# Kernel tuning notes

Hardware: AMD Instinct MI355X
Metric: run time of the kernel (lower is better)

Reference implementation:

```python
import jax, jax.numpy as jnp
import numpy as np

N_NODES = 50000
N_EDGES = 800000
IN_FEATS = 128
HIDDEN = 128
NUM_CLASSES = 47


def setup_inputs() -> dict:
    key = jax.random.key(0)
    k1, k2, k3, k4 = jax.random.split(key, 4)
    features = jax.random.normal(k1, (N_NODES, IN_FEATS), dtype=jnp.float32)
    edge_index = jax.random.randint(k2, (2, N_EDGES), 0, N_NODES, dtype=jnp.int32)
    # Glorot-style init for weights, zeros for bias (DGL GraphConv defaults)
    W1 = jax.random.normal(k3, (IN_FEATS, HIDDEN), dtype=jnp.float32) * (1.0 / np.sqrt(IN_FEATS))
    b1 = jnp.zeros((HIDDEN,), dtype=jnp.float32)
    W2 = jax.random.normal(k4, (HIDDEN, NUM_CLASSES), dtype=jnp.float32) * (1.0 / np.sqrt(HIDDEN))
    b2 = jnp.zeros((NUM_CLASSES,), dtype=jnp.float32)
    return {"features": features, "edge_index": edge_index,
            "W1": W1, "b1": b1, "W2": W2, "b2": b2}


def _graph_conv(x, W, b, src, dst, norm_src, norm_dst, n_nodes):
    # DGL GraphConv, norm='both': D_dst^{-1/2} A D_src^{-1/2} (X W) + b
    h = (x * norm_src[:, None]) @ W            # transform before aggregation
    agg = jax.ops.segment_sum(h[src], dst, num_segments=n_nodes)
    return agg * norm_dst[:, None] + b


def reference(features, edge_index, W1, b1, W2, b2):
    src, dst = edge_index[0], edge_index[1]
    n = features.shape[0]
    ones = jnp.ones((src.shape[0],), dtype=features.dtype)
    deg_out = jax.ops.segment_sum(ones, src, num_segments=n)
    deg_in = jax.ops.segment_sum(ones, dst, num_segments=n)
    norm_src = jax.lax.rsqrt(jnp.clip(deg_out, 1.0))   # d_out^{-1/2}, clamp >= 1
    norm_dst = jax.lax.rsqrt(jnp.clip(deg_in, 1.0))    # d_in^{-1/2}, clamp >= 1

    h = _graph_conv(features, W1, b1, src, dst, norm_src, norm_dst, n)
    h = jax.nn.relu(h)
    out = _graph_conv(h, W2, b2, src, dst, norm_src, norm_dst, n)
    return out
```

## Files before the change

### kernel.cpp

```cpp
#include <hip/hip_runtime.h>
#include <hip/hip_fp16.h>

#define N_NODES 50000
#define N_EDGES 800000
#define IN_F 128
#define HID 128
#define NCLS 47
#define H2S 48
#define W2C 64
#define NCH 196
#define TM 32
#define XTS 40
#define NB 64
#define CHUNK 12500
#define PDW 12500
#define HHALF 6250
#define FQ 3125
#define NHIST 256
#define MEGA_LDS 25088


struct __align__(8)  h2x2 { __half2 a, b; };
struct __align__(16) h2x4 { __half2 a, b, c, d; };

__global__ __launch_bounds__(256) void mega1_kernel(const int* __restrict__ ei,
                                                    unsigned int* __restrict__ Pdst,
                                                    unsigned int* __restrict__ Psrc,
                                                    const float* __restrict__ X,
                                                    const float* __restrict__ W1,
                                                    __half* __restrict__ H1h) {
    extern __shared__ __align__(16) char smem[];
    const int t = threadIdx.x;
    if (blockIdx.x < NHIST) {
        unsigned int* h = (unsigned int*)smem;
        const int job = blockIdx.x;
        const bool is_src = job >= NHIST / 2;
        const int half = (job >> 6) & 1;
        const int chunk = job & (NB - 1);
        const int* ids = is_src ? ei : ei + N_EDGES;
        uint2* h2 = (uint2*)h;
        for (int j = t; j < HHALF / 2; j += 256) h2[j] = make_uint2(0u, 0u);
        __syncthreads();
        const int e0 = chunk * CHUNK;
        const int lo = half * HHALF;
        for (int k = t; k < CHUNK; k += 256) {
            int v = ids[e0 + k];
            int rel = (v >> 2) - lo;
            if ((unsigned)rel < HHALF)
                atomicAdd(&h[rel], 1u << ((v & 3) * 8));
        }
        __syncthreads();
        unsigned int* P = (is_src ? Psrc : Pdst) + (size_t)chunk * PDW + lo;
        uint2* P2 = (uint2*)P;
        for (int j = t; j < HHALF / 2; j += 256) P2[j] = h2[j];
    } else {
        float* xs = (float*)smem;
        const int row0 = (blockIdx.x - NHIST) * TM;
#pragma unroll
        for (int i = 0; i < 4; ++i) {
            int id = t + 256 * i;
            int r = id & 31;
            int q = id >> 5;
            int row = row0 + r;
            float4 v = make_float4(0.f, 0.f, 0.f, 0.f);
            if (row < N_NODES) v = *(const float4*)&X[(size_t)row * IN_F + 4 * q];
            xs[(4 * q + 0) * XTS + r] = v.x;
            xs[(4 * q + 1) * XTS + r] = v.y;
            xs[(4 * q + 2) * XTS + r] = v.z;
            xs[(4 * q + 3) * XTS + r] = v.w;
        }
        __syncthreads();
        const int c = t & 31;
        const int rg = t >> 5;
        float acc[4][4] = {{0.f}};
#pragma unroll 4
        for (int k = 0; k < IN_F; ++k) {
            const float4 w4 = *(const float4*)&W1[k * HID + 4 * c];
            const float4 a4 = *(const float4*)&xs[k * XTS + 4 * rg];
            const float wv[4] = {w4.x, w4.y, w4.z, w4.w};
            const float av[4] = {a4.x, a4.y, a4.z, a4.w};
#pragma unroll
            for (int i = 0; i < 4; ++i)
#pragma unroll
                for (int j = 0; j < 4; ++j)
                    acc[i][j] += av[i] * wv[j];
        }
#pragma unroll
        for (int i = 0; i < 4; ++i) {
            int row = row0 + 4 * rg + i;
            if (row < N_NODES) {
                h2x2 p = {__floats2half2_rn(acc[i][0], acc[i][1]),
                          __floats2half2_rn(acc[i][2], acc[i][3])};
                *(h2x2*)&H1h[(size_t)row * HID + 4 * c] = p;
            }
        }
    }
}

__global__ __launch_bounds__(256) void reduce_kernel(unsigned int* __restrict__ Pdst,
                                                     const unsigned int* __restrict__ Psrc,
                                                     int* __restrict__ cnt_in,
                                                     float* __restrict__ norm_src,
                                                     float* __restrict__ norm_dst,
                                                     int* __restrict__ chunk_sums) {
    __shared__ int sm[256];
    const int t = threadIdx.x;
    const int j = blockIdx.x * 256 + t;
    int tot = 0;
    if (j < PDW) {
        unsigned int run = 0;
        for (int b = 0; b < NB; ++b) {
            unsigned int v = Pdst[(size_t)b * PDW + j];
            Pdst[(size_t)b * PDW + j] = run;
            run += v;
        }
        int n0 = run & 0xff, n1 = (run >> 8) & 0xff;
        int n2 = (run >> 16) & 0xff, n3 = (run >> 24) & 0xff;
        *(int4*)&cnt_in[4 * j] = make_int4(n0, n1, n2, n3);
        *(float4*)&norm_dst[4 * j] = make_float4(
            rsqrtf(fmaxf((float)n0, 1.0f)), rsqrtf(fmaxf((float)n1, 1.0f)),
            rsqrtf(fmaxf((float)n2, 1.0f)), rsqrtf(fmaxf((float)n3, 1.0f)));
        tot = n0 + n1 + n2 + n3;
        unsigned int rs = 0;
        for (int b = 0; b < NB; ++b) rs += Psrc[(size_t)b * PDW + j];
        int s0 = rs & 0xff, s1 = (rs >> 8) & 0xff;
        int s2 = (rs >> 16) & 0xff, s3 = (rs >> 24) & 0xff;
        *(float4*)&norm_src[4 * j] = make_float4(
            rsqrtf(fmaxf((float)s0, 1.0f)), rsqrtf(fmaxf((float)s1, 1.0f)),
            rsqrtf(fmaxf((float)s2, 1.0f)), rsqrtf(fmaxf((float)s3, 1.0f)));
    }
    sm[t] = tot;
    __syncthreads();
    const int g = t & 63;
    for (int off = 32; off > 0; off >>= 1) {
        if (g < off) sm[t] += sm[t + off];
        __syncthreads();
    }
    if (g == 0) chunk_sums[blockIdx.x * 4 + (t >> 6)] = sm[t];
}

__global__ __launch_bounds__(256) void scan3_kernel(const int* __restrict__ cnt_in,
                                                    const int* __restrict__ chunk_sums,
                                                    int* __restrict__ offsets,
                                                    const float* __restrict__ W2,
                                                    float* __restrict__ W2p) {
    __shared__ int sm[256];
    const int t = threadIdx.x;
    int v = (t < NCH) ? chunk_sums[t] : 0;
    sm[t] = v;
    __syncthreads();
    for (int off = 1; off < 256; off <<= 1) {
        int u = (t >= off) ? sm[t - off] : 0;
        __syncthreads();
        sm[t] += u;
        __syncthreads();
    }
    const int basev = (blockIdx.x == 0) ? 0 : sm[blockIdx.x - 1];
    __syncthreads();
    const int idx = blockIdx.x * 256 + t;
    int c = (idx < N_NODES) ? cnt_in[idx] : 0;
    sm[t] = c;
    __syncthreads();
    for (int off = 1; off < 256; off <<= 1) {
        int u = (t >= off) ? sm[t - off] : 0;
        __syncthreads();
        sm[t] += u;
        __syncthreads();
    }
    if (idx < N_NODES) offsets[idx] = basev + sm[t] - c;
    if (blockIdx.x == 0) {
        if (t == 0) offsets[N_NODES] = N_EDGES;
        for (int i2 = t; i2 < HID * W2C; i2 += 256) {
            int k = i2 >> 6, cc = i2 & 63;
            W2p[i2] = (cc < NCLS) ? W2[k * NCLS + cc] : 0.f;
        }
    }
}

__global__ __launch_bounds__(256) void fill_kernel(const int* __restrict__ src,
                                                   const int* __restrict__ dst,
                                                   const int* __restrict__ offsets,
                                                   const unsigned int* __restrict__ Pdst,
                                                   int* __restrict__ csr_src) {
    __shared__ unsigned int cur[FQ];
    const int quarter = blockIdx.x >> 6;
    const int chunk = blockIdx.x & (NB - 1);
    for (int j = threadIdx.x; j < FQ; j += 256) cur[j] = 0u;
    __syncthreads();
    const unsigned int* base = Pdst + (size_t)chunk * PDW;
    const int e0 = chunk * CHUNK;
    const int lo = quarter * FQ;
    for (int k = threadIdx.x; k < CHUNK; k += 256) {
        int d = dst[e0 + k];
        int rel = (d >> 2) - lo;
        if ((unsigned)rel < FQ) {
            const int sh = (d & 3) * 8;
            unsigned int old = atomicAdd(&cur[rel], 1u << sh);
            unsigned int rank = (old >> sh) & 0xffu;
            unsigned int bh = (base[d >> 2] >> sh) & 0xffu;
            csr_src[offsets[d] + (int)bh + (int)rank] = src[e0 + k];
        }
    }
}

__global__ __launch_bounds__(256) void gather1_kernel(const __half* __restrict__ H1h,
        const int* __restrict__ offsets, const int* __restrict__ csr_src,
        const float* __restrict__ b1, const float* __restrict__ norm_src,
        const float* __restrict__ norm_dst, __half* __restrict__ Hrelu16) {
    const int lane = threadIdx.x & 63;
    const int q = lane >> 4;
    const int fl = lane & 15;
    const int row = blockIdx.x * 4 + (threadIdx.x >> 6);
    const int beg = offsets[row], end = offsets[row + 1];
    float a0 = 0.f, a1 = 0.f, a2 = 0.f, a3 = 0.f;
    float a4 = 0.f, a5 = 0.f, a6 = 0.f, a7 = 0.f;
    for (int base = beg; base < end; base += 64) {
        int idx = 0;
        float nsv = 0.f;
        if (base + lane < end) {
            idx = csr_src[base + lane];
            nsv = norm_src[idx];
        }
        const int cnt = min(end - base, 64);
        for (int j = 0; j < cnt; j += 16) {
            int e0 = j + q, e1 = j + 4 + q, e2 = j + 8 + q, e3 = j + 12 + q;
            int s0 = __shfl(idx, e0);  float n0 = __shfl(nsv, e0);
            int s1 = __shfl(idx, e1);  float n1 = __shfl(nsv, e1);
            int s2 = __shfl(idx, e2);  float n2 = __shfl(nsv, e2);
            int s3 = __shfl(idx, e3);  float n3 = __shfl(nsv, e3);
            h2x4 v0 = *(const h2x4*)&H1h[(size_t)s0 * HID + 8 * fl];
            h2x4 v1 = *(const h2x4*)&H1h[(size_t)s1 * HID + 8 * fl];
            h2x4 v2 = *(const h2x4*)&H1h[(size_t)s2 * HID + 8 * fl];
            h2x4 v3 = *(const h2x4*)&H1h[(size_t)s3 * HID + 8 * fl];
            float2 f;
            f = __half22float2(v0.a); a0 = fmaf(f.x, n0, a0); a1 = fmaf(f.y, n0, a1);
            f = __half22float2(v0.b); a2 = fmaf(f.x, n0, a2); a3 = fmaf(f.y, n0, a3);
            f = __half22float2(v0.c); a4 = fmaf(f.x, n0, a4); a5 = fmaf(f.y, n0, a5);
            f = __half22float2(v0.d); a6 = fmaf(f.x, n0, a6); a7 = fmaf(f.y, n0, a7);
            f = __half22float2(v1.a); a0 = fmaf(f.x, n1, a0); a1 = fmaf(f.y, n1, a1);
            f = __half22float2(v1.b); a2 = fmaf(f.x, n1, a2); a3 = fmaf(f.y, n1, a3);
            f = __half22float2(v1.c); a4 = fmaf(f.x, n1, a4); a5 = fmaf(f.y, n1, a5);
            f = __half22float2(v1.d); a6 = fmaf(f.x, n1, a6); a7 = fmaf(f.y, n1, a7);
            f = __half22float2(v2.a); a0 = fmaf(f.x, n2, a0); a1 = fmaf(f.y, n2, a1);
            f = __half22float2(v2.b); a2 = fmaf(f.x, n2, a2); a3 = fmaf(f.y, n2, a3);
            f = __half22float2(v2.c); a4 = fmaf(f.x, n2, a4); a5 = fmaf(f.y, n2, a5);
            f = __half22float2(v2.d); a6 = fmaf(f.x, n2, a6); a7 = fmaf(f.y, n2, a7);
            f = __half22float2(v3.a); a0 = fmaf(f.x, n3, a0); a1 = fmaf(f.y, n3, a1);
            f = __half22float2(v3.b); a2 = fmaf(f.x, n3, a2); a3 = fmaf(f.y, n3, a3);
            f = __half22float2(v3.c); a4 = fmaf(f.x, n3, a4); a5 = fmaf(f.y, n3, a5);
            f = __half22float2(v3.d); a6 = fmaf(f.x, n3, a6); a7 = fmaf(f.y, n3, a7);
        }
    }
    a0 += __shfl_xor(a0, 16); a1 += __shfl_xor(a1, 16);
    a2 += __shfl_xor(a2, 16); a3 += __shfl_xor(a3, 16);
    a4 += __shfl_xor(a4, 16); a5 += __shfl_xor(a5, 16);
    a6 += __shfl_xor(a6, 16); a7 += __shfl_xor(a7, 16);
    a0 += __shfl_xor(a0, 32); a1 += __shfl_xor(a1, 32);
    a2 += __shfl_xor(a2, 32); a3 += __shfl_xor(a3, 32);
    a4 += __shfl_xor(a4, 32); a5 += __shfl_xor(a5, 32);
    a6 += __shfl_xor(a6, 32); a7 += __shfl_xor(a7, 32);
    if (lane < 16) {
        float nd = norm_dst[row], ns = norm_src[row];
        float4 bA = *(const float4*)&b1[8 * fl];
        float4 bB = *(const float4*)&b1[8 * fl + 4];
        float o0 = fmaxf(fmaf(a0, nd, bA.x), 0.f) * ns;
        float o1 = fmaxf(fmaf(a1, nd, bA.y), 0.f) * ns;
        float o2 = fmaxf(fmaf(a2, nd, bA.z), 0.f) * ns;
        float o3 = fmaxf(fmaf(a3, nd, bA.w), 0.f) * ns;
        float o4 = fmaxf(fmaf(a4, nd, bB.x), 0.f) * ns;
        float o5 = fmaxf(fmaf(a5, nd, bB.y), 0.f) * ns;
        float o6 = fmaxf(fmaf(a6, nd, bB.z), 0.f) * ns;
        float o7 = fmaxf(fmaf(a7, nd, bB.w), 0.f) * ns;
        h2x4 p = {__floats2half2_rn(o0, o1), __floats2half2_rn(o2, o3),
                  __floats2half2_rn(o4, o5), __floats2half2_rn(o6, o7)};
        *(h2x4*)&Hrelu16[(size_t)row * HID + 8 * fl] = p;
    }
}

__global__ __launch_bounds__(128) void gemm2_kernel(const __half* __restrict__ Hrelu16,
                                                    const float* __restrict__ W2p,
                                                    __half* __restrict__ H2h) {
    __shared__ __align__(16) float xs[HID * XTS];
    const int t = threadIdx.x;
    const int row0 = blockIdx.x * TM;
#pragma unroll
    for (int i = 0; i < 4; ++i) {
        int id = t + 128 * i;
        int r = id & 31;
        int g = id >> 5;
        int row = row0 + r;
        h2x4 v{};
        if (row < N_NODES) v = *(const h2x4*)&Hrelu16[(size_t)row * HID + 8 * g];
        float2 f0 = __half22float2(v.a), f1 = __half22float2(v.b);
        float2 f2 = __half22float2(v.c), f3 = __half22float2(v.d);
        xs[(8 * g + 0) * XTS + r] = f0.x;
        xs[(8 * g + 1) * XTS + r] = f0.y;
        xs[(8 * g + 2) * XTS + r] = f1.x;
        xs[(8 * g + 3) * XTS + r] = f1.y;
        xs[(8 * g + 4) * XTS + r] = f2.x;
        xs[(8 * g + 5) * XTS + r] = f2.y;
        xs[(8 * g + 6) * XTS + r] = f3.x;
        xs[(8 * g + 7) * XTS + r] = f3.y;
    }
    __syncthreads();
    const int c = t & 15;
    const int rg = t >> 4;
    float acc[4][4] = {{0.f}};
#pragma unroll 4
    for (int k = 0; k < HID; ++k) {
        const float4 w4 = *(const float4*)&W2p[k * W2C + 4 * c];
        const float4 a4 = *(const float4*)&xs[k * XTS + 4 * rg];
        const float wv[4] = {w4.x, w4.y, w4.z, w4.w};
        const float av[4] = {a4.x, a4.y, a4.z, a4.w};
#pragma unroll
        for (int i = 0; i < 4; ++i)
#pragma unroll
            for (int j = 0; j < 4; ++j)
                acc[i][j] += av[i] * wv[j];
    }
    if (c < 12) {
#pragma unroll
        for (int i = 0; i < 4; ++i) {
            int row = row0 + 4 * rg + i;
            if (row < N_NODES) {
                h2x2 p = {__floats2half2_rn(acc[i][0], acc[i][1]),
                          __floats2half2_rn(acc[i][2], acc[i][3])};
                *(h2x2*)&H2h[(size_t)row * H2S + 4 * c] = p;
            }
        }
    }
}

__global__ __launch_bounds__(256) void gather2_kernel(const __half* __restrict__ H2h,
        const int* __restrict__ offsets, const int* __restrict__ csr_src,
        const float* __restrict__ b2, const float* __restrict__ norm_dst,
        float* __restrict__ out) {
    const int lane = threadIdx.x & 63;
    const int row = blockIdx.x * 4 + (threadIdx.x >> 6);
    const int beg = offsets[row], end = offsets[row + 1];
    const int cl = min(lane, H2S - 1);
    float acc = 0.f;
    for (int base = beg; base < end; base += 64) {
        int idx = 0;
        float wv = 0.f;
        if (base + lane < end) {
            idx = csr_src[base + lane];
            wv = 1.f;
        }
        const int cnt = min(end - base, 64);
        for (int j = 0; j < cnt; j += 4) {
            int s0 = __shfl(idx, j);     float w0 = __shfl(wv, j);
            int s1 = __shfl(idx, j + 1); float w1 = __shfl(wv, j + 1);
            int s2 = __shfl(idx, j + 2); float w2 = __shfl(wv, j + 2);
            int s3 = __shfl(idx, j + 3); float w3 = __shfl(wv, j + 3);
            float f0 = __half2float(H2h[(size_t)s0 * H2S + cl]);
            float f1 = __half2float(H2h[(size_t)s1 * H2S + cl]);
            float f2 = __half2float(H2h[(size_t)s2 * H2S + cl]);
            float f3 = __half2float(H2h[(size_t)s3 * H2S + cl]);
            acc = fmaf(f0, w0, acc);
            acc = fmaf(f1, w1, acc);
            acc = fmaf(f2, w2, acc);
            acc = fmaf(f3, w3, acc);
        }
    }
    if (lane < NCLS) out[(size_t)row * NCLS + lane] = acc * norm_dst[row] + b2[lane];
}

extern "C" void kernel_launch(void* const* d_in, const int* in_sizes, int n_in,
                              void* d_out, int out_size, void* d_ws, size_t ws_size,
                              hipStream_t stream) {
    const float* X  = (const float*)d_in[0];
    const int*   ei = (const int*)d_in[1];
    const float* W1 = (const float*)d_in[2];
    const float* b1 = (const float*)d_in[3];
    const float* W2 = (const float*)d_in[4];
    const float* b2 = (const float*)d_in[5];
    float* out = (float*)d_out;

    const int* src = ei;
    const int* dst = ei + N_EDGES;

    char* w = (char*)d_ws;
    auto alloc = [&](size_t bytes) {
        char* p = w;
        w += (bytes + 255) & ~(size_t)255;
        return p;
    };
    float*  norm_src   = (float*)alloc(N_NODES * 4);
    float*  norm_dst   = (float*)alloc(N_NODES * 4);
    int*    cnt_in     = (int*)alloc(N_NODES * 4);
    int*    offsets    = (int*)alloc((N_NODES + 1) * 4);
    int*    csr_src    = (int*)alloc((size_t)N_EDGES * 4);
    int*    chunk_sums = (int*)alloc(NCH * 4);
    float*  W2p        = (float*)alloc((size_t)HID * W2C * 4);
    __half* H1h        = (__half*)alloc((size_t)N_NODES * HID * 2);
    __half* Hrelu16    = (__half*)alloc((size_t)N_NODES * HID * 2);
    __half* H2h        = (__half*)alloc((size_t)N_NODES * H2S * 2);
    unsigned int* Pdst = (unsigned int*)alloc((size_t)NB * PDW * 4);
    unsigned int* Psrc = (unsigned int*)alloc((size_t)NB * PDW * 4);

    const int gemm_blocks = (N_NODES + TM - 1) / TM;
    mega1_kernel<<<NHIST + gemm_blocks, 256, MEGA_LDS, stream>>>(ei, Pdst, Psrc,
                                                                 X, W1, H1h);
    reduce_kernel<<<(PDW + 255) / 256, 256, 0, stream>>>(Pdst, Psrc, cnt_in,
                                                         norm_src, norm_dst, chunk_sums);
    scan3_kernel<<<NCH, 256, 0, stream>>>(cnt_in, chunk_sums, offsets, W2, W2p);
    fill_kernel<<<4 * NB, 256, 0, stream>>>(src, dst, offsets, Pdst, csr_src);

    gather1_kernel<<<N_NODES / 4, 256, 0, stream>>>(H1h, offsets, csr_src, b1,
                                                    norm_src, norm_dst, Hrelu16);
    gemm2_kernel<<<gemm_blocks, 128, 0, stream>>>(Hrelu16, W2p, H2h);
    gather2_kernel<<<N_NODES / 4, 256, 0, stream>>>(H2h, offsets, csr_src, b2,
                                                    norm_dst, out);
}
```

Measured before the change: 240.8 us.

## Co-schedule GEMM1 with CSR fill instead of histogram, widen histogram blocks

Moves the first dense GEMM (X·W1 to fp16) out of the fused histogram kernel and into the CSR fill kernel, so the GEMM blocks run alongside the atomic-heavy fill phase instead of the histogram phase. The histogram becomes its own kernel using 512-thread blocks with static LDS. The aim is to better hide the latency-bound fill scatter behind compute and to let the short histogram launch finish faster. The risk is that fill blocks queued alongside many GEMM blocks may be delayed, and the fill kernel's LDS footprint grows to 20 KB.

```diff
diff --git a/kernel.cpp b/kernel.cpp
--- a/kernel.cpp
+++ b/kernel.cpp
@@ -17,84 +17,37 @@
 #define HHALF 6250
 #define FQ 3125
 #define NHIST 256
-#define MEGA_LDS 25088
+#define FG_LDS 20480
 
 
 struct __align__(8)  h2x2 { __half2 a, b; };
 struct __align__(16) h2x4 { __half2 a, b, c, d; };
 
-__global__ __launch_bounds__(256) void mega1_kernel(const int* __restrict__ ei,
-                                                    unsigned int* __restrict__ Pdst,
-                                                    unsigned int* __restrict__ Psrc,
-                                                    const float* __restrict__ X,
-                                                    const float* __restrict__ W1,
-                                                    __half* __restrict__ H1h) {
-    extern __shared__ __align__(16) char smem[];
+__global__ __launch_bounds__(512) void hist_kernel(const int* __restrict__ ei,
+                                                   unsigned int* __restrict__ Pdst,
+                                                   unsigned int* __restrict__ Psrc) {
+    __shared__ unsigned int h[HHALF];
     const int t = threadIdx.x;
-    if (blockIdx.x < NHIST) {
-        unsigned int* h = (unsigned int*)smem;
-        const int job = blockIdx.x;
-        const bool is_src = job >= NHIST / 2;
-        const int half = (job >> 6) & 1;
-        const int chunk = job & (NB - 1);
-        const int* ids = is_src ? ei : ei + N_EDGES;
-        uint2* h2 = (uint2*)h;
-        for (int j = t; j < HHALF / 2; j += 256) h2[j] = make_uint2(0u, 0u);
-        __syncthreads();
-        const int e0 = chunk * CHUNK;
-        const int lo = half * HHALF;
-        for (int k = t; k < CHUNK; k += 256) {
-            int v = ids[e0 + k];
-            int rel = (v >> 2) - lo;
-            if ((unsigned)rel < HHALF)
-                atomicAdd(&h[rel], 1u << ((v & 3) * 8));
-        }
-        __syncthreads();
-        unsigned int* P = (is_src ? Psrc : Pdst) + (size_t)chunk * PDW + lo;
-        uint2* P2 = (uint2*)P;
-        for (int j = t; j < HHALF / 2; j += 256) P2[j] = h2[j];
-    } else {
-        float* xs = (float*)smem;
-        const int row0 = (blockIdx.x - NHIST) * TM;
-#pragma unroll
-        for (int i = 0; i < 4; ++i) {
-            int id = t + 256 * i;
-            int r = id & 31;
-            int q = id >> 5;
-            int row = row0 + r;
-            float4 v = make_float4(0.f, 0.f, 0.f, 0.f);
-            if (row < N_NODES) v = *(const float4*)&X[(size_t)row * IN_F + 4 * q];
-            xs[(4 * q + 0) * XTS + r] = v.x;
-            xs[(4 * q + 1) * XTS + r] = v.y;
-            xs[(4 * q + 2) * XTS + r] = v.z;
-            xs[(4 * q + 3) * XTS + r] = v.w;
-        }
-        __syncthreads();
-        const int c = t & 31;
-        const int rg = t >> 5;
-        float acc[4][4] = {{0.f}};
-#pragma unroll 4
-        for (int k = 0; k < IN_F; ++k) {
-            const float4 w4 = *(const float4*)&W1[k * HID + 4 * c];
-            const float4 a4 = *(const float4*)&xs[k * XTS + 4 * rg];
-            const float wv[4] = {w4.x, w4.y, w4.z, w4.w};
-            const float av[4] = {a4.x, a4.y, a4.z, a4.w};
-#pragma unroll
-            for (int i = 0; i < 4; ++i)
-#pragma unroll
-                for (int j = 0; j < 4; ++j)
-                    acc[i][j] += av[i] * wv[j];
-        }
-#pragma unroll
-        for (int i = 0; i < 4; ++i) {
-            int row = row0 + 4 * rg + i;
-            if (row < N_NODES) {
-                h2x2 p = {__floats2half2_rn(acc[i][0], acc[i][1]),
-                          __floats2half2_rn(acc[i][2], acc[i][3])};
-                *(h2x2*)&H1h[(size_t)row * HID + 4 * c] = p;
-            }
-        }
-    }
+    const int job = blockIdx.x;
+    const bool is_src = job >= NHIST / 2;
+    const int half = (job >> 6) & 1;
+    const int chunk = job & (NB - 1);
+    const int* ids = is_src ? ei : ei + N_EDGES;
+    uint2* h2 = (uint2*)h;
+    for (int j = t; j < HHALF / 2; j += 512) h2[j] = make_uint2(0u, 0u);
+    __syncthreads();
+    const int e0 = chunk * CHUNK;
+    const int lo = half * HHALF;
+    for (int k = t; k < CHUNK; k += 512) {
+        int v = ids[e0 + k];
+        int rel = (v >> 2) - lo;
+        if ((unsigned)rel < HHALF)
+            atomicAdd(&h[rel], 1u << ((v & 3) * 8));
+    }
+    __syncthreads();
+    unsigned int* P = (is_src ? Psrc : Pdst) + (size_t)chunk * PDW + lo;
+    uint2* P2 = (uint2*)P;
+    for (int j = t; j < HHALF / 2; j += 512) P2[j] = h2[j];
 }
 
 __global__ __launch_bounds__(256) void reduce_kernel(unsigned int* __restrict__ Pdst,
@@ -177,28 +130,73 @@
     }
 }
 
-__global__ __launch_bounds__(256) void fill_kernel(const int* __restrict__ src,
-                                                   const int* __restrict__ dst,
-                                                   const int* __restrict__ offsets,
-                                                   const unsigned int* __restrict__ Pdst,
-                                                   int* __restrict__ csr_src) {
-    __shared__ unsigned int cur[FQ];
-    const int quarter = blockIdx.x >> 6;
-    const int chunk = blockIdx.x & (NB - 1);
-    for (int j = threadIdx.x; j < FQ; j += 256) cur[j] = 0u;
-    __syncthreads();
-    const unsigned int* base = Pdst + (size_t)chunk * PDW;
-    const int e0 = chunk * CHUNK;
-    const int lo = quarter * FQ;
-    for (int k = threadIdx.x; k < CHUNK; k += 256) {
-        int d = dst[e0 + k];
-        int rel = (d >> 2) - lo;
-        if ((unsigned)rel < FQ) {
-            const int sh = (d & 3) * 8;
-            unsigned int old = atomicAdd(&cur[rel], 1u << sh);
-            unsigned int rank = (old >> sh) & 0xffu;
-            unsigned int bh = (base[d >> 2] >> sh) & 0xffu;
-            csr_src[offsets[d] + (int)bh + (int)rank] = src[e0 + k];
+__global__ __launch_bounds__(256) void fill_gemm1_kernel(const int* __restrict__ src,
+        const int* __restrict__ dst, const int* __restrict__ offsets,
+        const unsigned int* __restrict__ Pdst, int* __restrict__ csr_src,
+        const float* __restrict__ X, const float* __restrict__ W1,
+        __half* __restrict__ H1h) {
+    __shared__ __align__(16) char smem[FG_LDS];
+    const int t = threadIdx.x;
+    if (blockIdx.x < 4 * NB) {
+        unsigned int* cur = (unsigned int*)smem;
+        const int quarter = blockIdx.x >> 6;
+        const int chunk = blockIdx.x & (NB - 1);
+        for (int j = t; j < FQ; j += 256) cur[j] = 0u;
+        __syncthreads();
+        const unsigned int* base = Pdst + (size_t)chunk * PDW;
+        const int e0 = chunk * CHUNK;
+        const int lo = quarter * FQ;
+        for (int k = t; k < CHUNK; k += 256) {
+            int d = dst[e0 + k];
+            int rel = (d >> 2) - lo;
+            if ((unsigned)rel < FQ) {
+                const int sh = (d & 3) * 8;
+                unsigned int old = atomicAdd(&cur[rel], 1u << sh);
+                unsigned int rank = (old >> sh) & 0xffu;
+                unsigned int bh = (base[d >> 2] >> sh) & 0xffu;
+                csr_src[offsets[d] + (int)bh + (int)rank] = src[e0 + k];
+            }
+        }
+    } else {
+        float* xs = (float*)smem;
+        const int row0 = (blockIdx.x - 4 * NB) * TM;
+#pragma unroll
+        for (int i = 0; i < 4; ++i) {
+            int id = t + 256 * i;
+            int r = id & 31;
+            int q = id >> 5;
+            int row = row0 + r;
+            float4 v = make_float4(0.f, 0.f, 0.f, 0.f);
+            if (row < N_NODES) v = *(const float4*)&X[(size_t)row * IN_F + 4 * q];
+            xs[(4 * q + 0) * XTS + r] = v.x;
+            xs[(4 * q + 1) * XTS + r] = v.y;
+            xs[(4 * q + 2) * XTS + r] = v.z;
+            xs[(4 * q + 3) * XTS + r] = v.w;
+        }
+        __syncthreads();
+        const int c = t & 31;
+        const int rg = t >> 5;
+        float acc[4][4] = {{0.f}};
+#pragma unroll 4
+        for (int k = 0; k < IN_F; ++k) {
+            const float4 w4 = *(const float4*)&W1[k * HID + 4 * c];
+            const float4 a4 = *(const float4*)&xs[k * XTS + 4 * rg];
+            const float wv[4] = {w4.x, w4.y, w4.z, w4.w};
+            const float av[4] = {a4.x, a4.y, a4.z, a4.w};
+#pragma unroll
+            for (int i = 0; i < 4; ++i)
+#pragma unroll
+                for (int j = 0; j < 4; ++j)
+                    acc[i][j] += av[i] * wv[j];
+        }
+#pragma unroll
+        for (int i = 0; i < 4; ++i) {
+            int row = row0 + 4 * rg + i;
+            if (row < N_NODES) {
+                h2x2 p = {__floats2half2_rn(acc[i][0], acc[i][1]),
+                          __floats2half2_rn(acc[i][2], acc[i][3])};
+                *(h2x2*)&H1h[(size_t)row * HID + 4 * c] = p;
+            }
         }
     }
 }
@@ -400,13 +398,13 @@
     unsigned int* Psrc = (unsigned int*)alloc((size_t)NB * PDW * 4);
 
     const int gemm_blocks = (N_NODES + TM - 1) / TM;
-    mega1_kernel<<<NHIST + gemm_blocks, 256, MEGA_LDS, stream>>>(ei, Pdst, Psrc,
-                                                                 X, W1, H1h);
+    hist_kernel<<<NHIST, 512, 0, stream>>>(ei, Pdst, Psrc);
     reduce_kernel<<<(PDW + 255) / 256, 256, 0, stream>>>(Pdst, Psrc, cnt_in,
                                                          norm_src, norm_dst, chunk_sums);
     scan3_kernel<<<NCH, 256, 0, stream>>>(cnt_in, chunk_sums, offsets, W2, W2p);
-    fill_kernel<<<4 * NB, 256, 0, stream>>>(src, dst, offsets, Pdst, csr_src);
-
+    fill_gemm1_kernel<<<4 * NB + gemm_blocks, 256, 0, stream>>>(src, dst, offsets,
+                                                                Pdst, csr_src,
+                                                                X, W1, H1h);
     gather1_kernel<<<N_NODES / 4, 256, 0, stream>>>(H1h, offsets, csr_src, b1,
                                                     norm_src, norm_dst, Hrelu16);
     gemm2_kernel<<<gemm_blocks, 128, 0, stream>>>(Hrelu16, W2p, H2h);
```

After: 218.8 us. 1.1x faster.
